# Kernel tuning notes

Measured on AMD Instinct MI355X. Metric: run time of the kernel, lower is better.

The kernel has to match this reference:

```python
import jax, jax.numpy as jnp
import numpy as np

D = 512      # model_channels
H = 4        # heads
L = 4        # num_transfomers_layers
DK = D // H
EPS = 1e-5


def inorm(x):
    # nn.InstanceNorm1d(d_model) applied to (bs, seq, d_model): normalizes over
    # the last (d_model) axis per token, no affine params.
    m = jnp.mean(x, axis=-1, keepdims=True)
    v = jnp.var(x, axis=-1, keepdims=True)
    return (x - m) * jax.lax.rsqrt(v + EPS)


def mha(xq, xkv, w, b, mask):
    # w: [4, D, D] (q,k,v,out), b: [4, D]; mask: [bs,S,S] (1 = masked)
    bs, S, _ = xq.shape
    q = (xq @ w[0] + b[0]).reshape(bs, S, H, DK).transpose(0, 2, 1, 3)
    k = (xkv @ w[1] + b[1]).reshape(bs, S, H, DK).transpose(0, 2, 1, 3)
    v = (xkv @ w[2] + b[2]).reshape(bs, S, H, DK).transpose(0, 2, 1, 3)
    scores = jnp.einsum('bhqd,bhkd->bhqk', q, k) / jnp.sqrt(jnp.float32(DK))
    scores = jnp.where(mask[:, None] == 1, jnp.float32(-1e9), scores)
    attn = jax.nn.softmax(scores, axis=-1)
    out = jnp.einsum('bhqk,bhkd->bhqd', attn, v)
    out = out.transpose(0, 2, 1, 3).reshape(bs, S, D)
    return out @ w[3] + b[3]


def setup_inputs() -> dict:
    key = jax.random.key(0)
    ks = jax.random.split(key, 24)
    bs, S = 16, 512
    sc = 0.02
    inp = {
        'x': jax.random.normal(ks[0], (bs, S, 18), jnp.float32),
        'cond': jax.random.normal(ks[1], (bs, S, 89), jnp.float32),
        'door_mask': jax.random.randint(ks[2], (bs, S, S), 0, 2, jnp.int32),
        'self_mask': jax.random.randint(ks[3], (bs, S, S), 0, 2, jnp.int32),
        'gen_mask': jax.random.randint(ks[4], (bs, S, S), 0, 2, jnp.int32),
        # attention params: [L, 3 branches (door,self,gen), 4 projs (q,k,v,out)]
        'attn_w': jax.random.normal(ks[5], (L, 3, 4, D, D), jnp.float32) * sc,
        'attn_b': jnp.zeros((L, 3, 4, D), jnp.float32),
        'ff_w1': jax.random.normal(ks[6], (L, D, 2 * D), jnp.float32) * sc,
        'ff_b1': jnp.zeros((L, 2 * D), jnp.float32),
        'ff_w2': jax.random.normal(ks[7], (L, 2 * D, D), jnp.float32) * sc,
        'ff_b2': jnp.zeros((L, D), jnp.float32),
        'in_w': jax.random.normal(ks[8], (18, D), jnp.float32) * sc,
        'in_b': jnp.zeros((D,), jnp.float32),
        'cond_w': jax.random.normal(ks[9], (89, D), jnp.float32) * sc,
        'cond_b': jnp.zeros((D,), jnp.float32),
        'out1_w': jax.random.normal(ks[10], (D, D), jnp.float32) * sc,
        'out1_b': jnp.zeros((D,), jnp.float32),
        'out2_w': jax.random.normal(ks[11], (D, D // 2), jnp.float32) * sc,
        'out2_b': jnp.zeros((D // 2,), jnp.float32),
        'out3_w': jax.random.normal(ks[12], (D // 2, 2), jnp.float32) * sc,
        'out3_b': jnp.zeros((2,), jnp.float32),
    }
    return inp


def reference(x, cond, door_mask, self_mask, gen_mask,
              attn_w, attn_b, ff_w1, ff_b1, ff_w2, ff_b2,
              in_w, in_b, cond_w, cond_b,
              out1_w, out1_b, out2_w, out2_b, out3_w, out3_b):
    h = (x @ in_w + in_b) + (cond @ cond_w + cond_b)  # [bs,S,D]
    for l in range(L):
        h2 = inorm(h)
        h = (h
             + mha(h2, h2, attn_w[l, 0], attn_b[l, 0], door_mask)
             + mha(h2, h2, attn_w[l, 1], attn_b[l, 1], self_mask)
             + mha(h2, h2, attn_w[l, 2], attn_b[l, 2], gen_mask))
        h2 = inorm(h)
        h = h + jax.nn.relu(h2 @ ff_w1[l] + ff_b1[l]) @ ff_w2[l] + ff_b2[l]
    out = jax.nn.relu(h @ out1_w + out1_b)
    out = jax.nn.relu(out @ out2_w + out2_b)
    out = out @ out3_w + out3_b  # [bs,S,2]
    return out
```

## Files before the change

### kernel.cpp

```cpp
#include <hip/hip_runtime.h>
#include <hip/hip_bf16.h>

#define DEV static __device__ __forceinline__

typedef __attribute__((ext_vector_type(8))) short bfx8;
typedef __attribute__((ext_vector_type(4))) float f32x4;
typedef __attribute__((ext_vector_type(4))) unsigned short us4;

DEV unsigned short f2bf(float f){
  unsigned u = __builtin_bit_cast(unsigned, f);
  u += 0x7fffu + ((u >> 16) & 1u);
  return (unsigned short)(u >> 16);
}
DEV float bf2f(unsigned short h){
  unsigned u = ((unsigned)h) << 16;
  return __builtin_bit_cast(float, u);
}
DEV void gld16(const void* g, void* l){
  __builtin_amdgcn_global_load_lds((const __attribute__((address_space(1))) void*)g,
                                   (__attribute__((address_space(3))) void*)l, 16, 0, 0);
}
DEV f32x4 mfma16(bfx8 a, bfx8 b, f32x4 c){
  return __builtin_amdgcn_mfma_f32_16x16x32_bf16(a, b, c, 0, 0, 0);
}

__global__ __launch_bounds__(256, 2)
void wconv_kernel(const float* __restrict__ attn_w, const float* __restrict__ ff_w1,
                  const float* __restrict__ ff_w2, const float* __restrict__ out1_w,
                  const float* __restrict__ out2_w,
                  unsigned short* __restrict__ bqkv, unsigned short* __restrict__ bout,
                  unsigned short* __restrict__ bff1, unsigned short* __restrict__ bff2,
                  unsigned short* __restrict__ bo1, unsigned short* __restrict__ bo2)
{
  __shared__ float ts[64][65];
  const int z = blockIdx.z;
  const float* src; unsigned short* dst; int K, N, stride;
  if (z < 48){
    int l = z / 12, br = (z % 12) >> 2, p = z & 3;
    src = attn_w + (size_t)z * 262144; K = 512; N = 512;
    if (p < 3){ dst = bqkv + (size_t)l * 4608 * 512 + (size_t)(br * 3 + p) * 262144; stride = 512; }
    else      { dst = bout + (size_t)l * 512 * 1536 + (size_t)br * 512;              stride = 1536; }
  } else if (z < 52){
    int l = z - 48; src = ff_w1 + (size_t)l * 524288; K = 512; N = 1024;
    dst = bff1 + (size_t)l * 524288; stride = 512;
  } else if (z < 56){
    int l = z - 52; src = ff_w2 + (size_t)l * 524288; K = 1024; N = 512;
    dst = bff2 + (size_t)l * 524288; stride = 1024;
  } else if (z == 56){
    src = out1_w; K = 512; N = 512; dst = bo1; stride = 512;
  } else {
    src = out2_w; K = 512; N = 256; dst = bo2; stride = 512;
  }
  const int n0 = blockIdx.x << 6, k0 = blockIdx.y << 6;
  if (n0 >= N || k0 >= K) return;
  const int tx = threadIdx.x & 63, ty = threadIdx.x >> 6;
  #pragma unroll
  for (int i = 0; i < 16; ++i){
    int row = (ty << 4) + i;
    ts[row][tx] = src[(size_t)(k0 + row) * N + n0 + tx];
  }
  __syncthreads();
  #pragma unroll
  for (int i = 0; i < 16; ++i){
    int row = (ty << 4) + i;
    dst[(size_t)(n0 + row) * stride + k0 + tx] = f2bf(ts[tx][row]);
  }
}

__global__ __launch_bounds__(256, 4)
void embed_kernel(const float* __restrict__ x, const float* __restrict__ cond,
                  const float* __restrict__ in_w, const float* __restrict__ in_b,
                  const float* __restrict__ cond_w, const float* __restrict__ cond_b,
                  float* __restrict__ h)
{
  __shared__ float xs[18];
  __shared__ float cs[89];
  const int m = blockIdx.x;
  const int tid = threadIdx.x;
  if (tid < 18) xs[tid] = x[(size_t)m * 18 + tid];
  if (tid >= 32 && tid < 121) cs[tid - 32] = cond[(size_t)m * 89 + (tid - 32)];
  __syncthreads();
  #pragma unroll
  for (int hf = 0; hf < 2; ++hf){
    const int c = tid + (hf << 8);
    float a = in_b[c] + cond_b[c];
    #pragma unroll
    for (int k = 0; k < 18; ++k) a += xs[k] * in_w[k * 512 + c];
    for (int k = 0; k < 89; ++k) a += cs[k] * cond_w[k * 512 + c];
    h[(size_t)m * 512 + c] = a;
  }
}

__global__ __launch_bounds__(256, 4)
void inorm_kernel(const float* __restrict__ in, unsigned short* __restrict__ ob)
{
  const int wid = (blockIdx.x << 2) + (threadIdx.x >> 6);
  const int lane = threadIdx.x & 63;
  const float* row = in + (size_t)wid * 512;
  const float4 v0 = *(const float4*)(row + (lane << 2));
  const float4 v1 = *(const float4*)(row + 256 + (lane << 2));
  float s = v0.x + v0.y + v0.z + v0.w + v1.x + v1.y + v1.z + v1.w;
  float q = v0.x*v0.x + v0.y*v0.y + v0.z*v0.z + v0.w*v0.w
          + v1.x*v1.x + v1.y*v1.y + v1.z*v1.z + v1.w*v1.w;
  #pragma unroll
  for (int sh = 1; sh < 64; sh <<= 1){
    s += __shfl_xor(s, sh, 64);
    q += __shfl_xor(q, sh, 64);
  }
  const float mean = s * (1.f / 512.f);
  const float var = q * (1.f / 512.f) - mean * mean;
  const float rs = rsqrtf(var + 1e-5f);
  us4 o0, o1;
  o0[0] = f2bf((v0.x - mean) * rs); o0[1] = f2bf((v0.y - mean) * rs);
  o0[2] = f2bf((v0.z - mean) * rs); o0[3] = f2bf((v0.w - mean) * rs);
  o1[0] = f2bf((v1.x - mean) * rs); o1[1] = f2bf((v1.y - mean) * rs);
  o1[2] = f2bf((v1.z - mean) * rs); o1[3] = f2bf((v1.w - mean) * rs);
  *(us4*)(ob + (size_t)wid * 512 + (lane << 2)) = o0;
  *(us4*)(ob + (size_t)wid * 512 + 256 + (lane << 2)) = o1;
}

__global__ void f2b_kernel(const float* __restrict__ in, unsigned short* __restrict__ ob, int n)
{
  const int i = (blockIdx.x * 256 + threadIdx.x) << 2;
  if (i >= n) return;
  const float4 v = *(const float4*)(in + i);
  us4 o; o[0] = f2bf(v.x); o[1] = f2bf(v.y); o[2] = f2bf(v.z); o[3] = f2bf(v.w);
  *(us4*)(ob + i) = o;
}

template<int MODE>
__global__ __launch_bounds__(256, 2)
void gemm_bt(const unsigned short* __restrict__ A, const unsigned short* __restrict__ B,
             const float* __restrict__ bias, float* __restrict__ Cf,
             unsigned short* __restrict__ Cb, unsigned short* __restrict__ qkp,
             unsigned short* __restrict__ vtp, int M, int N, int K)
{
  __shared__ unsigned short As[128 * 64];
  __shared__ unsigned short Bs[128 * 64];
  const int tid = threadIdx.x;
  const int w = tid >> 6, lane = tid & 63;
  const int wm = w >> 1, wn = w & 1;
  const int lr = lane & 15, lh = lane >> 4;
  const int m0 = blockIdx.x << 7, n0 = blockIdx.y << 7;
  const int rA = lane >> 3;
  const int cA = (lane & 7) << 3;

  f32x4 acc[4][4];
  #pragma unroll
  for (int i = 0; i < 4; ++i)
    #pragma unroll
    for (int j = 0; j < 4; ++j) acc[i][j] = (f32x4)0.f;

  const int nkt = K >> 6;
  auto stage = [&](int kt){
    #pragma unroll
    for (int c = 0; c < 4; ++c){
      const int r = (c << 5) + (w << 3) + rA;
      gld16(A + (size_t)(m0 + r) * K + (kt << 6) + cA,
            (char*)As + ((c << 5) + (w << 3)) * 128);
      gld16(B + (size_t)(n0 + r) * K + (kt << 6) + cA,
            (char*)Bs + ((c << 5) + (w << 3)) * 128);
    }
  };
  stage(0);
  for (int kt = 0; kt < nkt; ++kt){
    __syncthreads();
    #pragma unroll
    for (int kk = 0; kk < 2; ++kk){
      bfx8 af[4], bg[4];
      #pragma unroll
      for (int i = 0; i < 4; ++i)
        af[i] = *(const bfx8*)(As + ((wm << 6) + (i << 4) + lr) * 64 + (kk << 5) + (lh << 3));
      #pragma unroll
      for (int j = 0; j < 4; ++j)
        bg[j] = *(const bfx8*)(Bs + ((wn << 6) + (j << 4) + lr) * 64 + (kk << 5) + (lh << 3));
      #pragma unroll
      for (int i = 0; i < 4; ++i)
        #pragma unroll
        for (int j = 0; j < 4; ++j)
          acc[i][j] = mfma16(af[i], bg[j], acc[i][j]);
    }
    __syncthreads();
    if (kt + 1 < nkt) stage(kt + 1);
  }
  #pragma unroll
  for (int i = 0; i < 4; ++i){
    const int row = m0 + (wm << 6) + (i << 4) + (lh << 2);
    #pragma unroll
    for (int j = 0; j < 4; ++j){
      const int col = n0 + (wn << 6) + (j << 4) + lr;
      if constexpr (MODE == 1){
        const float bv = bias ? bias[col] : 0.f;
        #pragma unroll
        for (int r = 0; r < 4; ++r){
          float v = acc[i][j][r] + bv;
          v = fmaxf(v, 0.f);
          Cb[(size_t)(row + r) * N + col] = f2bf(v);
        }
      } else if constexpr (MODE == 2){
        const float bv = bias ? bias[col] : 0.f;
        #pragma unroll
        for (int r = 0; r < 4; ++r){
          const size_t idx = (size_t)(row + r) * N + col;
          Cf[idx] += acc[i][j][r] + bv;
        }
      } else {
        const int br = col / 1536;
        const int rem = col - br * 1536;
        const int p = rem >> 9;
        const int c = rem & 511;
        const float bv = bias ? bias[(size_t)((br << 2) + p) * 512 + c] : 0.f;
        if (p < 2){
          #pragma unroll
          for (int r = 0; r < 4; ++r)
            qkp[((size_t)((br << 1) + p) * 8192 + row + r) * 512 + c] = f2bf(acc[i][j][r] + bv);
        } else {
          const int b_ = row >> 9, s0 = row & 511;
          const int hi = c >> 7, dk = c & 127;
          us4 pk;
          #pragma unroll
          for (int r = 0; r < 4; ++r) pk[r] = f2bf(acc[i][j][r] + bv);
          *(us4*)(vtp + (((size_t)(br * 16 + b_) * 4 + hi) * 128 + dk) * 512 + s0) = pk;
        }
      }
    }
  }
}

__global__ __launch_bounds__(256, 2)
void attn_kernel(const unsigned short* __restrict__ qk, const unsigned short* __restrict__ vt,
                 const int* __restrict__ mask0, const int* __restrict__ mask1,
                 const int* __restrict__ mask2, unsigned short* __restrict__ outp)
{
  __shared__ unsigned short Pl[4 * 16 * 512];
  __shared__ unsigned short Ks[32 * 128];
  __shared__ unsigned short Vs[128 * 32];
  const int tid = threadIdx.x;
  const int w = tid >> 6, lane = tid & 63;
  const int lr = lane & 15, lh = lane >> 4;
  const int qt = blockIdx.x, bh = blockIdx.y, br = blockIdx.z;
  const int b = bh >> 2, h = bh & 3;
  const int q0 = (qt << 6) + (w << 4);
  const int* mask = (br == 0) ? mask0 : ((br == 1) ? mask1 : mask2);
  const int* mrow = mask + (size_t)b * 512 * 512;

  const unsigned short* qbase = qk + ((size_t)(br * 2 + 0) * 8192 + (size_t)b * 512) * 512 + h * 128;
  const unsigned short* kbase = qk + ((size_t)(br * 2 + 1) * 8192 + (size_t)b * 512) * 512 + h * 128;
  const unsigned short* vbase = vt + ((size_t)(br * 16 + b) * 4 + h) * 128 * 512;

  bfx8 aq[4];
  #pragma unroll
  for (int t = 0; t < 4; ++t)
    aq[t] = *(const bfx8*)(qbase + (size_t)(q0 + lr) * 512 + (t << 5) + (lh << 3));

  f32x4 sc[16][2];
  const float scale = 0.08838834764831845f;

  const int krow = (w << 2) + (lane >> 4);
  const int kcol = (lane & 15) << 3;
  const int vrow = (w << 4) + (lane >> 2);
  const int vcol = (lane & 3) << 3;

  #pragma unroll
  for (int kt = 0; kt < 16; ++kt){
    __syncthreads();
    #pragma unroll
    for (int c2 = 0; c2 < 2; ++c2){
      gld16(kbase + (size_t)((kt << 5) + (c2 << 4) + krow) * 512 + kcol,
            (char*)Ks + ((c2 << 4) + (w << 2)) * 256);
    }
    __syncthreads();
    #pragma unroll
    for (int j = 0; j < 2; ++j){
      f32x4 a2 = (f32x4)0.f;
      #pragma unroll
      for (int t = 0; t < 4; ++t){
        bfx8 bk = *(const bfx8*)(Ks + ((j << 4) + lr) * 128 + (t << 5) + (lh << 3));
        a2 = mfma16(aq[t], bk, a2);
      }
      #pragma unroll
      for (int r = 0; r < 4; ++r){
        const int q = q0 + (lh << 2) + r;
        const int kcl = (kt << 5) + (j << 4) + lr;
        const int mv = mrow[(size_t)q * 512 + kcl];
        sc[kt][j][r] = mv ? -1e9f : a2[r] * scale;
      }
    }
  }

  float mx[4] = {-3e38f, -3e38f, -3e38f, -3e38f};
  #pragma unroll
  for (int kt = 0; kt < 16; ++kt)
    #pragma unroll
    for (int j = 0; j < 2; ++j)
      #pragma unroll
      for (int r = 0; r < 4; ++r) mx[r] = fmaxf(mx[r], sc[kt][j][r]);
  #pragma unroll
  for (int s = 1; s < 16; s <<= 1)
    #pragma unroll
    for (int r = 0; r < 4; ++r) mx[r] = fmaxf(mx[r], __shfl_xor(mx[r], s, 64));
  float sm[4] = {0.f, 0.f, 0.f, 0.f};
  unsigned short* pw = Pl + (w << 13);
  #pragma unroll
  for (int kt = 0; kt < 16; ++kt)
    #pragma unroll
    for (int j = 0; j < 2; ++j)
      #pragma unroll
      for (int r = 0; r < 4; ++r){
        const int q = (lh << 2) + r;
        const int kcl = (kt << 5) + (j << 4) + lr;
        const float pv = __expf(sc[kt][j][r] - mx[r]);
        sm[r] += pv;
        pw[(q << 9) + (kcl ^ ((q & 7) << 3))] = f2bf(pv);
      }
  #pragma unroll
  for (int s = 1; s < 16; s <<= 1)
    #pragma unroll
    for (int r = 0; r < 4; ++r) sm[r] += __shfl_xor(sm[r], s, 64);
  float linv[4];
  #pragma unroll
  for (int r = 0; r < 4; ++r) linv[r] = 1.f / sm[r];

  f32x4 ao[8];
  #pragma unroll
  for (int j = 0; j < 8; ++j) ao[j] = (f32x4)0.f;
  #pragma unroll
  for (int kt = 0; kt < 16; ++kt){
    __syncthreads();
    #pragma unroll
    for (int c2 = 0; c2 < 2; ++c2){
      gld16(vbase + (size_t)((c2 << 6) + vrow) * 512 + (kt << 5) + vcol,
            (char*)Vs + ((c2 << 6) + (w << 4)) * 64);
    }
    __syncthreads();
    bfx8 pa = *(const bfx8*)(pw + (lr << 9) + (((kt << 5) + (lh << 3)) ^ ((lr & 7) << 3)));
    #pragma unroll
    for (int j = 0; j < 8; ++j){
      bfx8 bv = *(const bfx8*)(Vs + ((j << 4) + lr) * 32 + (lh << 3));
      ao[j] = mfma16(pa, bv, ao[j]);
    }
  }
  const size_t obase = (size_t)(b * 512) * 1536 + br * 512 + h * 128;
  #pragma unroll
  for (int j = 0; j < 8; ++j){
    const int d = (j << 4) + lr;
    #pragma unroll
    for (int r = 0; r < 4; ++r){
      const int q = q0 + (lh << 2) + r;
      outp[obase + (size_t)q * 1536 + d] = f2bf(ao[j][r] * linv[r]);
    }
  }
}

__global__ __launch_bounds__(256, 4)
void out3_kernel(const unsigned short* __restrict__ t2, const float* __restrict__ w,
                 const float* __restrict__ b2, float* __restrict__ outp)
{
  const int row = (blockIdx.x << 2) + (threadIdx.x >> 6);
  const int lane = threadIdx.x & 63;
  const unsigned short* rp = t2 + (size_t)row * 256 + (lane << 2);
  float a0 = 0.f, a1 = 0.f;
  #pragma unroll
  for (int k = 0; k < 4; ++k){
    const float v = bf2f(rp[k]);
    const int kk = (lane << 2) + k;
    a0 += v * w[kk * 2 + 0];
    a1 += v * w[kk * 2 + 1];
  }
  #pragma unroll
  for (int s = 1; s < 64; s <<= 1){
    a0 += __shfl_xor(a0, s, 64);
    a1 += __shfl_xor(a1, s, 64);
  }
  if (lane == 0){
    outp[(size_t)row * 2 + 0] = a0 + b2[0];
    outp[(size_t)row * 2 + 1] = a1 + b2[1];
  }
}

extern "C" void kernel_launch(void* const* d_in, const int* in_sizes, int n_in,
                              void* d_out, int out_size, void* d_ws, size_t ws_size,
                              hipStream_t stream)
{
  const float* x      = (const float*)d_in[0];
  const float* cond   = (const float*)d_in[1];
  const int*   mdoor  = (const int*)d_in[2];
  const int*   mself  = (const int*)d_in[3];
  const int*   mgen   = (const int*)d_in[4];
  const float* attn_w = (const float*)d_in[5];
  const float* attn_b = (const float*)d_in[6];
  const float* ff_w1  = (const float*)d_in[7];
  const float* ff_b1  = (const float*)d_in[8];
  const float* ff_w2  = (const float*)d_in[9];
  const float* ff_b2  = (const float*)d_in[10];
  const float* in_w   = (const float*)d_in[11];
  const float* in_b   = (const float*)d_in[12];
  const float* cond_w = (const float*)d_in[13];
  const float* cond_b = (const float*)d_in[14];
  const float* out1_w = (const float*)d_in[15];
  const float* out1_b = (const float*)d_in[16];
  const float* out2_w = (const float*)d_in[17];
  const float* out2_b = (const float*)d_in[18];
  const float* out3_w = (const float*)d_in[19];
  const float* out3_b = (const float*)d_in[20];

  char* p = (char*)d_ws;
  auto carve = [&](size_t bytes) -> char* {
    char* r = p; p += (bytes + 255) & ~(size_t)255; return r;
  };
  float*          h    = (float*)carve(8192ull * 512 * 4);
  unsigned short* h2   = (unsigned short*)carve(8192ull * 512 * 2);
  unsigned short* bqkv = (unsigned short*)carve(4ull * 4608 * 512 * 2);
  unsigned short* bout = (unsigned short*)carve(4ull * 512 * 1536 * 2);
  unsigned short* bff1 = (unsigned short*)carve(4ull * 1024 * 512 * 2);
  unsigned short* bff2 = (unsigned short*)carve(4ull * 512 * 1024 * 2);
  unsigned short* bo1  = (unsigned short*)carve(512ull * 512 * 2);
  unsigned short* bo2  = (unsigned short*)carve(256ull * 512 * 2);
  unsigned short* qkb  = (unsigned short*)carve(6ull * 8192 * 512 * 2);
  unsigned short* vtb  = (unsigned short*)carve(3ull * 16 * 4 * 128 * 512 * 2);
  unsigned short* att  = (unsigned short*)carve(8192ull * 1536 * 2);
  unsigned short* t    = (unsigned short*)carve(8192ull * 1024 * 2);
  unsigned short* t2   = (unsigned short*)carve(8192ull * 256 * 2);
  float* outf = (float*)d_out;

  wconv_kernel<<<dim3(16, 16, 58), 256, 0, stream>>>(attn_w, ff_w1, ff_w2, out1_w, out2_w,
                                                     bqkv, bout, bff1, bff2, bo1, bo2);
  embed_kernel<<<dim3(8192), 256, 0, stream>>>(x, cond, in_w, in_b, cond_w, cond_b, h);
  for (int l = 0; l < 4; ++l){
    inorm_kernel<<<dim3(2048), 256, 0, stream>>>(h, h2);
    gemm_bt<3><<<dim3(64, 36), 256, 0, stream>>>(h2, bqkv + (size_t)l * 4608 * 512,
        attn_b + (size_t)l * 6144, nullptr, nullptr, qkb, vtb, 8192, 4608, 512);
    attn_kernel<<<dim3(8, 64, 3), 256, 0, stream>>>(qkb, vtb, mdoor, mself, mgen, att);
    gemm_bt<2><<<dim3(64, 4), 256, 0, stream>>>(att, bout + (size_t)l * 512 * 1536,
        nullptr, h, nullptr, nullptr, nullptr, 8192, 512, 1536);
    inorm_kernel<<<dim3(2048), 256, 0, stream>>>(h, h2);
    gemm_bt<1><<<dim3(64, 8), 256, 0, stream>>>(h2, bff1 + (size_t)l * 1024 * 512,
        ff_b1 + (size_t)l * 1024, nullptr, t, nullptr, nullptr, 8192, 1024, 512);
    gemm_bt<2><<<dim3(64, 4), 256, 0, stream>>>(t, bff2 + (size_t)l * 512 * 1024,
        ff_b2 + (size_t)l * 512, h, nullptr, nullptr, nullptr, 8192, 512, 1024);
  }
  f2b_kernel<<<dim3(4096), 256, 0, stream>>>(h, h2, 8192 * 512);
  gemm_bt<1><<<dim3(64, 4), 256, 0, stream>>>(h2, bo1, out1_b, nullptr, att, nullptr, nullptr, 8192, 512, 512);
  gemm_bt<1><<<dim3(64, 2), 256, 0, stream>>>(att, bo2, out2_b, nullptr, t2, nullptr, nullptr, 8192, 256, 512);
  out3_kernel<<<dim3(2048), 256, 0, stream>>>(t2, out3_w, out3_b, outf);
}
```

Measured before the change: 1.348 ms.

## Bit-pack masks once, double-buffer K/V with swizzled LDS in attention

Adds a kernel that packs the three int32 attention masks into bitmasks once per call, so the four attention launches read 1 bit per element through LDS instead of 4-byte global loads. The attention kernel double-buffers K and V tiles with XOR-swizzled LDS layouts to overlap loads and reduce bank conflicts. It keeps the softmax probabilities in registers, staging only a small per-tile P slice, and remaps the grid so blocks sharing a branch and head are spread across it. The cost is an extra pack kernel and higher register pressure from holding probabilities longer.

```diff
diff --git a/kernel.cpp b/kernel.cpp
--- a/kernel.cpp
+++ b/kernel.cpp
@@ -64,6 +64,23 @@
   for (int i = 0; i < 16; ++i){
     int row = (ty << 4) + i;
     dst[(size_t)(n0 + row) * stride + k0 + tx] = f2bf(ts[tx][row]);
+  }
+}
+
+__global__ __launch_bounds__(256, 4)
+void mpack_kernel(const int* __restrict__ m0, const int* __restrict__ m1,
+                  const int* __restrict__ m2, unsigned long long* __restrict__ mp)
+{
+  const int row = (blockIdx.x << 2) + (threadIdx.x >> 6);
+  const int lane = threadIdx.x & 63;
+  const int* src = (row < 8192) ? (m0 + (size_t)row * 512)
+                 : (row < 16384 ? (m1 + (size_t)(row - 8192) * 512)
+                                : (m2 + (size_t)(row - 16384) * 512));
+  #pragma unroll
+  for (int c = 0; c < 8; ++c){
+    const int v = src[(c << 6) + lane];
+    const unsigned long long b = __ballot(v != 0);
+    if (lane == c) mp[(size_t)row * 8 + c] = b;
   }
 }
 
@@ -229,24 +246,30 @@
 
 __global__ __launch_bounds__(256, 2)
 void attn_kernel(const unsigned short* __restrict__ qk, const unsigned short* __restrict__ vt,
-                 const int* __restrict__ mask0, const int* __restrict__ mask1,
-                 const int* __restrict__ mask2, unsigned short* __restrict__ outp)
-{
-  __shared__ unsigned short Pl[4 * 16 * 512];
-  __shared__ unsigned short Ks[32 * 128];
-  __shared__ unsigned short Vs[128 * 32];
+                 const unsigned* __restrict__ mp, unsigned short* __restrict__ outp)
+{
+  __shared__ unsigned short KV[2][4096];
+  __shared__ unsigned short Pl[4][16 * 40];
+  __shared__ unsigned Mk[64 * 17];
   const int tid = threadIdx.x;
   const int w = tid >> 6, lane = tid & 63;
   const int lr = lane & 15, lh = lane >> 4;
-  const int qt = blockIdx.x, bh = blockIdx.y, br = blockIdx.z;
+  const int id = blockIdx.x;
+  const int pair = (id & 7) * 192 / 8 + ((id >> 3) >> 3);
+  const int qt = (id >> 3) & 7;
+  const int br = pair >> 6, bh = pair & 63;
   const int b = bh >> 2, h = bh & 3;
   const int q0 = (qt << 6) + (w << 4);
-  const int* mask = (br == 0) ? mask0 : ((br == 1) ? mask1 : mask2);
-  const int* mrow = mask + (size_t)b * 512 * 512;
 
   const unsigned short* qbase = qk + ((size_t)(br * 2 + 0) * 8192 + (size_t)b * 512) * 512 + h * 128;
   const unsigned short* kbase = qk + ((size_t)(br * 2 + 1) * 8192 + (size_t)b * 512) * 512 + h * 128;
   const unsigned short* vbase = vt + ((size_t)(br * 16 + b) * 4 + h) * 128 * 512;
+  const unsigned* mrow = mp + ((size_t)br * 8192 + (size_t)b * 512 + (qt << 6)) * 16;
+
+  for (int idx = tid; idx < 1024; idx += 256){
+    const int rw = idx >> 4, wd = idx & 15;
+    Mk[rw * 17 + wd] = mrow[rw * 16 + wd];
+  }
 
   bfx8 aq[4];
   #pragma unroll
@@ -256,34 +279,48 @@
   f32x4 sc[16][2];
   const float scale = 0.08838834764831845f;
 
-  const int krow = (w << 2) + (lane >> 4);
-  const int kcol = (lane & 15) << 3;
-  const int vrow = (w << 4) + (lane >> 2);
-  const int vcol = (lane & 3) << 3;
-
-  #pragma unroll
+  auto stageK = [&](int kt){
+    char* dst = (char*)KV[kt & 1];
+    #pragma unroll
+    for (int c2 = 0; c2 < 2; ++c2){
+      const int trow = (c2 << 4) + (w << 2) + (lane >> 4);
+      const int g = (lane & 15) ^ (trow & 7);
+      gld16(kbase + (size_t)((kt << 5) + trow) * 512 + (g << 3),
+            dst + ((c2 << 4) + (w << 2)) * 256);
+    }
+  };
+  auto stageV = [&](int kt){
+    char* dst = (char*)KV[kt & 1];
+    #pragma unroll
+    for (int c2 = 0; c2 < 2; ++c2){
+      const int drow = (c2 << 6) + (w << 4) + (lane >> 2);
+      const int g = (lane & 3) ^ (drow & 3);
+      gld16(vbase + (size_t)drow * 512 + (kt << 5) + (g << 3),
+            dst + ((c2 << 6) + (w << 4)) * 64);
+    }
+  };
+
+  stageK(0);
   for (int kt = 0; kt < 16; ++kt){
     __syncthreads();
-    #pragma unroll
-    for (int c2 = 0; c2 < 2; ++c2){
-      gld16(kbase + (size_t)((kt << 5) + (c2 << 4) + krow) * 512 + kcol,
-            (char*)Ks + ((c2 << 4) + (w << 2)) * 256);
-    }
-    __syncthreads();
+    if (kt < 15) stageK(kt + 1);
+    const unsigned short* Ksb = KV[kt & 1];
     #pragma unroll
     for (int j = 0; j < 2; ++j){
+      const int rk = (j << 4) + lr;
       f32x4 a2 = (f32x4)0.f;
       #pragma unroll
       for (int t = 0; t < 4; ++t){
-        bfx8 bk = *(const bfx8*)(Ks + ((j << 4) + lr) * 128 + (t << 5) + (lh << 3));
+        const int s = ((t << 2) + lh) ^ (rk & 7);
+        bfx8 bk = *(const bfx8*)(Ksb + rk * 128 + (s << 3));
         a2 = mfma16(aq[t], bk, a2);
       }
       #pragma unroll
       for (int r = 0; r < 4; ++r){
-        const int q = q0 + (lh << 2) + r;
-        const int kcl = (kt << 5) + (j << 4) + lr;
-        const int mv = mrow[(size_t)q * 512 + kcl];
-        sc[kt][j][r] = mv ? -1e9f : a2[r] * scale;
+        const int qloc = (w << 4) + (lh << 2) + r;
+        const unsigned mword = Mk[qloc * 17 + kt];
+        const int bit = (mword >> ((j << 4) + lr)) & 1;
+        sc[kt][j][r] = bit ? -1e9f : a2[r] * scale;
       }
     }
   }
@@ -300,18 +337,15 @@
     #pragma unroll
     for (int r = 0; r < 4; ++r) mx[r] = fmaxf(mx[r], __shfl_xor(mx[r], s, 64));
   float sm[4] = {0.f, 0.f, 0.f, 0.f};
-  unsigned short* pw = Pl + (w << 13);
   #pragma unroll
   for (int kt = 0; kt < 16; ++kt)
     #pragma unroll
     for (int j = 0; j < 2; ++j)
       #pragma unroll
       for (int r = 0; r < 4; ++r){
-        const int q = (lh << 2) + r;
-        const int kcl = (kt << 5) + (j << 4) + lr;
         const float pv = __expf(sc[kt][j][r] - mx[r]);
+        sc[kt][j][r] = pv;
         sm[r] += pv;
-        pw[(q << 9) + (kcl ^ ((q & 7) << 3))] = f2bf(pv);
       }
   #pragma unroll
   for (int s = 1; s < 16; s <<= 1)
@@ -324,19 +358,24 @@
   f32x4 ao[8];
   #pragma unroll
   for (int j = 0; j < 8; ++j) ao[j] = (f32x4)0.f;
-  #pragma unroll
+  unsigned short* pw = Pl[w];
+  __syncthreads();
+  stageV(0);
   for (int kt = 0; kt < 16; ++kt){
     __syncthreads();
-    #pragma unroll
-    for (int c2 = 0; c2 < 2; ++c2){
-      gld16(vbase + (size_t)((c2 << 6) + vrow) * 512 + (kt << 5) + vcol,
-            (char*)Vs + ((c2 << 6) + (w << 4)) * 64);
-    }
-    __syncthreads();
-    bfx8 pa = *(const bfx8*)(pw + (lr << 9) + (((kt << 5) + (lh << 3)) ^ ((lr & 7) << 3)));
+    if (kt < 15) stageV(kt + 1);
+    #pragma unroll
+    for (int j = 0; j < 2; ++j)
+      #pragma unroll
+      for (int r = 0; r < 4; ++r)
+        pw[((lh << 2) + r) * 40 + (j << 4) + lr] = f2bf(sc[kt][j][r] * linv[r]);
+    bfx8 pa = *(const bfx8*)(pw + lr * 40 + (lh << 3));
+    const unsigned short* Vsb = KV[kt & 1];
     #pragma unroll
     for (int j = 0; j < 8; ++j){
-      bfx8 bv = *(const bfx8*)(Vs + ((j << 4) + lr) * 32 + (lh << 3));
+      const int dd = (j << 4) + lr;
+      const int s = lh ^ (dd & 3);
+      bfx8 bv = *(const bfx8*)(Vsb + dd * 32 + (s << 3));
       ao[j] = mfma16(pa, bv, ao[j]);
     }
   }
@@ -347,7 +386,7 @@
     #pragma unroll
     for (int r = 0; r < 4; ++r){
       const int q = q0 + (lh << 2) + r;
-      outp[obase + (size_t)q * 1536 + d] = f2bf(ao[j][r] * linv[r]);
+      outp[obase + (size_t)q * 1536 + d] = f2bf(ao[j][r]);
     }
   }
 }
@@ -421,16 +460,18 @@
   unsigned short* att  = (unsigned short*)carve(8192ull * 1536 * 2);
   unsigned short* t    = (unsigned short*)carve(8192ull * 1024 * 2);
   unsigned short* t2   = (unsigned short*)carve(8192ull * 256 * 2);
+  unsigned long long* mpk = (unsigned long long*)carve(24576ull * 8 * 8);
   float* outf = (float*)d_out;
 
   wconv_kernel<<<dim3(16, 16, 58), 256, 0, stream>>>(attn_w, ff_w1, ff_w2, out1_w, out2_w,
                                                      bqkv, bout, bff1, bff2, bo1, bo2);
+  mpack_kernel<<<dim3(6144), 256, 0, stream>>>(mdoor, mself, mgen, mpk);
   embed_kernel<<<dim3(8192), 256, 0, stream>>>(x, cond, in_w, in_b, cond_w, cond_b, h);
   for (int l = 0; l < 4; ++l){
     inorm_kernel<<<dim3(2048), 256, 0, stream>>>(h, h2);
     gemm_bt<3><<<dim3(64, 36), 256, 0, stream>>>(h2, bqkv + (size_t)l * 4608 * 512,
         attn_b + (size_t)l * 6144, nullptr, nullptr, qkb, vtb, 8192, 4608, 512);
-    attn_kernel<<<dim3(8, 64, 3), 256, 0, stream>>>(qkb, vtb, mdoor, mself, mgen, att);
+    attn_kernel<<<dim3(1536), 256, 0, stream>>>(qkb, vtb, (const unsigned*)mpk, att);
     gemm_bt<2><<<dim3(64, 4), 256, 0, stream>>>(att, bout + (size_t)l * 512 * 1536,
         nullptr, h, nullptr, nullptr, nullptr, 8192, 512, 1536);
     inorm_kernel<<<dim3(2048), 256, 0, stream>>>(h, h2);
```

Result: faster. 1.298 ms (-3.7%).
